# Optimization experiments

Hardware: AMD Instinct MI355X
Metric: run time of the kernel (lower is better)

Reference implementation:

```python
import jax, jax.numpy as jnp
import numpy as np

WS = 8            # window size (square)
HEADS = 16
HEAD_DIM = 32
DIM = 512
NEG_INF = float('-inf')


def _create_mask(ws, disp, upper_lower, left_right):
    size = ws * ws
    m = np.zeros((size, size), dtype=np.float32)
    d = disp
    if upper_lower:
        m[-d * ws:, :-d * ws] = NEG_INF
        m[:-d * ws, -d * ws:] = NEG_INF
    if left_right:
        m = m.reshape(ws, ws, ws, ws)
        m[:, -d:, :, :-d] = NEG_INF
        m[:, :-d, :, -d:] = NEG_INF
        m = m.reshape(size, size)
    return m


def _relative_indices(ws):
    coords = np.array([[x, y] for x in range(ws) for y in range(ws)])  # [ws^2, 2]
    dist = coords[None, :, :] - coords[:, None, :]                      # [ws^2, ws^2, 2]
    dist += ws - 1
    return dist.astype(np.int64)


_REL_IDX = _relative_indices(WS)                      # [64, 64, 2]
_UL_MASK = jnp.asarray(_create_mask(WS, WS // 2, True, False))   # [64, 64]
_LR_MASK = jnp.asarray(_create_mask(WS, WS // 2, False, True))   # [64, 64]


def setup_inputs() -> dict:
    key = jax.random.key(0)
    ks = jax.random.split(key, 5)
    b, n = 16, 64
    return {
        'x': jax.random.normal(ks[0], (b, n, n, DIM), dtype=jnp.float32),
        'w_qkv': jax.random.normal(ks[1], (3 * HEADS * HEAD_DIM, DIM), dtype=jnp.float32) * 0.02,
        'pos_embedding': jax.random.normal(ks[2], (2 * WS - 1, 2 * WS - 1), dtype=jnp.float32),
        'w_out': jax.random.normal(ks[3], (DIM, HEADS * HEAD_DIM), dtype=jnp.float32) * 0.02,
        'b_out': jax.random.normal(ks[4], (DIM,), dtype=jnp.float32) * 0.02,
    }


def reference(x, w_qkv, pos_embedding, w_out, b_out):
    disp = WS // 2
    scale = HEAD_DIM ** -0.5
    b, n_h, n_w, _ = x.shape
    nw_h, nw_w = n_h // WS, n_w // WS

    # cyclic shift (shifted=True)
    x = jnp.roll(x, shift=(-disp, -disp), axis=(1, 2))

    qkv = x @ w_qkv.T                                   # [b, n_h, n_w, 3*h*d]
    qkv = qkv.reshape(b, nw_h, WS, nw_w, WS, 3, HEADS, HEAD_DIM)
    # -> [3, b, heads, n_windows, window_tokens, head_dim]
    qkv = qkv.transpose(5, 0, 6, 1, 3, 2, 4, 7).reshape(
        3, b, HEADS, nw_h * nw_w, WS * WS, HEAD_DIM)
    q, k, v = qkv[0], qkv[1], qkv[2]

    dots = jnp.einsum('bhwid,bhwjd->bhwij', q, k) * scale
    # relative position bias
    dots = dots + pos_embedding[_REL_IDX[:, :, 0], _REL_IDX[:, :, 1]]
    # shift masks: last window-row and last window-column
    dots = dots.at[:, :, -nw_w:].add(_UL_MASK)
    dots = dots.at[:, :, nw_w - 1::nw_w].add(_LR_MASK)

    attn = jax.nn.softmax(dots, axis=-1)
    out = jnp.einsum('bhwij,bhwjd->bhwid', attn, v)     # [b,h,nw,ws^2,d]

    out = out.reshape(b, HEADS, nw_h, nw_w, WS, WS, HEAD_DIM)
    out = out.transpose(0, 2, 4, 3, 5, 1, 6).reshape(b, n_h, n_w, HEADS * HEAD_DIM)
    out = out @ w_out.T + b_out

    out = jnp.roll(out, shift=(disp, disp), axis=(1, 2))
    return out
```

## Files before the change

kernel.cpp:

```cpp
#include <hip/hip_runtime.h>
#include <hip/hip_bf16.h>
#include <stdint.h>

typedef __bf16 bf16;
typedef __attribute__((ext_vector_type(4))) float f32x4;
typedef __attribute__((ext_vector_type(8))) bf16 bf16x8;
typedef __attribute__((ext_vector_type(4))) bf16 bf16x4;

#define AS1 __attribute__((address_space(1)))
#define AS3 __attribute__((address_space(3)))

static __device__ __forceinline__ void gload_lds16(const bf16* g, bf16* l) {
  __builtin_amdgcn_global_load_lds((const AS1 void*)g, (AS3 void*)l, 16, 0, 0);
}

#define BAR __builtin_amdgcn_s_barrier()
#define LGKM0 asm volatile("s_waitcnt lgkmcnt(0)" ::: "memory")
#define VMC(n) asm volatile("s_waitcnt vmcnt(" #n ")" ::: "memory")
#define SCHED0 __builtin_amdgcn_sched_barrier(0)

#define STAGE_A(gsrc, dst, kt_) do {                                          \
  _Pragma("unroll") for (int s_ = 0; s_ < 4; ++s_) {                          \
    int idx_ = s_ * 256 + tid;                                                \
    int r_ = idx_ >> 3, c_ = idx_ & 7;                                        \
    gload_lds16((gsrc) + (size_t)r_ * 512 + ((kt_) << 6) + ((c_ ^ (r_ & 7)) << 3), \
                (dst) + idx_ * 8);                                            \
  }                                                                           \
} while (0)

#define LOADB(ktq, NCOLX) do {                                                \
  const bf16* bp_ = Bptr + (size_t)(ktq) * ((size_t)(NCOLX) * 64);            \
  _Pragma("unroll") for (int cb_ = 0; cb_ < 4; ++cb_)                         \
  _Pragma("unroll") for (int ks_ = 0; ks_ < 2; ++ks_)                         \
    bfr[cb_][ks_] = *(const bf16x8*)(bp_ + cb_ * 128 + (size_t)ks_ * (NCOLX) * 32); \
} while (0)

#define LOADB6(ktq) do {                                                      \
  const bf16* bp_ = Bptr + (size_t)(ktq) * 98304;                             \
  _Pragma("unroll") for (int cb_ = 0; cb_ < 6; ++cb_)                         \
  _Pragma("unroll") for (int ks_ = 0; ks_ < 2; ++ks_)                         \
    bfr[cb_][ks_] = *(const bf16x8*)(bp_ + cb_ * 128 + ks_ * 49152);          \
} while (0)

#define KLOOP_BD(Ag, NCOLX)                                                   \
  f32x4 acc[4][4] = {};                                                       \
  bf16x8 af[4][2], bfr[4][2];                                                 \
  STAGE_A(Ag, SA0, 0);                                                        \
  LOADB(0, NCOLX);                                                            \
  VMC(8); BAR;                                                                \
  STAGE_A(Ag, SA1, 1);                                                        \
  _Pragma("unroll 2")                                                         \
  for (int kt = 0; kt < 8; ++kt) {                                            \
    bf16* Ap = (kt & 1) ? SA1 : SA0;                                          \
    _Pragma("unroll") for (int i_ = 0; i_ < 4; ++i_) {                        \
      int ra_ = wr + i_ * 16 + lr;                                            \
      _Pragma("unroll") for (int ks_ = 0; ks_ < 2; ++ks_)                     \
        af[i_][ks_] = *(const bf16x8*)(Ap + ra_ * 64 + (((ks_ * 4 + lg) ^ (ra_ & 7)) << 3)); \
    }                                                                         \
    LGKM0; SCHED0;                                                            \
    __builtin_amdgcn_s_setprio(1);                                            \
    _Pragma("unroll") for (int i_ = 0; i_ < 4; ++i_)                          \
    _Pragma("unroll") for (int j_ = 0; j_ < 4; ++j_)                          \
    _Pragma("unroll") for (int ks_ = 0; ks_ < 2; ++ks_)                       \
      acc[i_][j_] = __builtin_amdgcn_mfma_f32_16x16x32_bf16(                  \
          af[i_][ks_], bfr[j_][ks_], acc[i_][j_], 0, 0, 0);                   \
    __builtin_amdgcn_s_setprio(0);                                            \
    if (kt < 7) LOADB(kt + 1, NCOLX);                                         \
    if (kt < 7) { VMC(8); }                                                   \
    BAR;                                                                      \
    if (kt < 6) STAGE_A(Ag, Ap, kt + 2);                                      \
  }

__global__ __launch_bounds__(256) void prep_x(const float* __restrict__ x,
                                              bf16* __restrict__ xs) {
  int m = blockIdx.x * 8 + (threadIdx.x >> 5);
  int lane = threadIdx.x & 31;
  int b = m >> 12, win = (m >> 6) & 63, t = m & 63;
  int ip = ((win >> 3) << 3) + (t >> 3);
  int jp = ((win & 7) << 3) + (t & 7);
  int io = (ip + 4) & 63, jo = (jp + 4) & 63;
  const float* src = x + ((((size_t)(b << 6) + io) << 6) + jo) * 512;
  bf16* dst = xs + ((size_t)m << 9);
  #pragma unroll
  for (int c0 = 0; c0 < 512; c0 += 128) {
    int c = c0 + lane * 4;
    float4 v = *(const float4*)(src + c);
    bf16x4 o = { (bf16)v.x, (bf16)v.y, (bf16)v.z, (bf16)v.w };
    *(bf16x4*)(dst + c) = o;
  }
}

__global__ __launch_bounds__(256) void prep_w(const float* __restrict__ wqkv,
                                              const float* __restrict__ wout,
                                              bf16* __restrict__ wqkv_bt,
                                              bf16* __restrict__ wout_bt) {
  int r = blockIdx.x * 8 + (threadIdx.x >> 5);
  int lane = threadIdx.x & 31;
  const float* src;
  bf16* dstb;
  int ncol, col;
  float sc = 1.0f;
  if (r < 1536) {
    int part = r >> 9, h = (r >> 5) & 15, d = r & 31;
    src = wqkv + (size_t)r * 512; dstb = wqkv_bt; ncol = 1536;
    col = h * 96 + part * 32 + d;
    if (part == 0) sc = 0.17677669529663689f;
  } else {
    src = wout + (size_t)(r - 1536) * 512; dstb = wout_bt; ncol = 512; col = r - 1536;
  }
  #pragma unroll
  for (int kb = lane; kb < 64; kb += 32) {
    float4 v0 = *(const float4*)(src + kb * 8);
    float4 v1 = *(const float4*)(src + kb * 8 + 4);
    bf16x8 o = { (bf16)(v0.x * sc), (bf16)(v0.y * sc), (bf16)(v0.z * sc), (bf16)(v0.w * sc),
                 (bf16)(v1.x * sc), (bf16)(v1.y * sc), (bf16)(v1.z * sc), (bf16)(v1.w * sc) };
    *(bf16x8*)(dstb + ((size_t)kb * ncol + col) * 8) = o;
  }
}

__global__ __launch_bounds__(256) void prep_bias(const float* __restrict__ pos,
                                                 float* __restrict__ bias4) {
  for (int idx = threadIdx.x; idx < 4 * 4096; idx += 256) {
    int ty = idx >> 12, ij = idx & 4095;
    int i = ij >> 6, j = ij & 63;
    int rx = ((j >> 3) - (i >> 3)) + 7;
    int ry = ((j & 7) - (i & 7)) + 7;
    float v = pos[rx * 15 + ry];
    if ((ty & 1) && (((i ^ j) >> 5) & 1)) v = -1e30f;
    if ((ty & 2) && (((i ^ j) >> 2) & 1)) v = -1e30f;
    bias4[idx] = v;
  }
}

__global__ __launch_bounds__(256, 2) void qkv_attn(
    const bf16* __restrict__ xs, const bf16* __restrict__ wb2,
    const float* __restrict__ bias4, bf16* __restrict__ ao) {
  __shared__ union { bf16 A[2][8192]; bf16 E[4][4096]; } sm;
  bf16* SA0 = sm.A[0]; bf16* SA1 = sm.A[1];

  const int tid = threadIdx.x, wave = tid >> 6, lane = tid & 63;
  const int ww = wave & 1, wh = wave >> 1;
  const int lr = lane & 15, lg = lane >> 4;

  int bid = blockIdx.x;
  bid = (bid & 7) * 512 + (bid >> 3);
  const int mt = bid >> 3, hp = bid & 7;
  const int h = hp * 2 + wh;

  const bf16* Ag = xs + ((size_t)mt * 128) * 512;
  const bf16* Bptr = wb2 + (((size_t)lg * 1536) + h * 96 + lr) * 8;

  f32x4 acc[4][6] = {};
  bf16x8 af[4][2], bfr[6][2];

  STAGE_A(Ag, SA0, 0);
  LOADB6(0);
  VMC(12); BAR;
  STAGE_A(Ag, SA1, 1);
  #pragma unroll 2
  for (int kt = 0; kt < 8; ++kt) {
    bf16* Ap = (kt & 1) ? SA1 : SA0;
    #pragma unroll
    for (int i_ = 0; i_ < 4; ++i_) {
      int ra_ = ww * 64 + i_ * 16 + lr;
      #pragma unroll
      for (int ks_ = 0; ks_ < 2; ++ks_)
        af[i_][ks_] = *(const bf16x8*)(Ap + ra_ * 64 + (((ks_ * 4 + lg) ^ (ra_ & 7)) << 3));
    }
    LGKM0; SCHED0;
    __builtin_amdgcn_s_setprio(1);
    #pragma unroll
    for (int i_ = 0; i_ < 4; ++i_)
      #pragma unroll
      for (int j_ = 0; j_ < 6; ++j_)
        #pragma unroll
        for (int ks_ = 0; ks_ < 2; ++ks_)
          acc[i_][j_] = __builtin_amdgcn_mfma_f32_16x16x32_bf16(
              af[i_][ks_], bfr[j_][ks_], acc[i_][j_], 0, 0, 0);
    __builtin_amdgcn_s_setprio(0);
    if (kt < 7) { LOADB6(kt + 1); VMC(12); }
    BAR;
    if (kt < 6) STAGE_A(Ag, Ap, kt + 2);
  }
  bf16* Ew = sm.E[wave];
  #pragma unroll
  for (int i = 0; i < 4; ++i)
    #pragma unroll
    for (int r = 0; r < 4; ++r) {
      int row = i * 16 + (lg << 2) + r;
      #pragma unroll
      for (int j = 0; j < 4; ++j) {
        int c = j * 16 + lr;
        Ew[row * 64 + (c ^ ((row & 7) << 3))] = (bf16)acc[i][j][r];
      }
    }
  bf16x8 vf[2][2];
  {
    const int s0 = lr + 16 * ((2 * lg) & 3);
    const int s1 = lr + 16 * ((2 * lg + 1) & 3);
    const bool lo = (lg < 2);
    #pragma unroll
    for (int kk = 0; kk < 2; ++kk)
      #pragma unroll
      for (int nj = 0; nj < 2; ++nj) {
        float f[8];
        #pragma unroll
        for (int c = 0; c < 4; ++c) {
          float a0 = __shfl(acc[2 * kk][4 + nj][c], s0);
          float a1 = __shfl(acc[2 * kk + 1][4 + nj][c], s0);
          f[c] = lo ? a0 : a1;
          float b0 = __shfl(acc[2 * kk][4 + nj][c], s1);
          float b1 = __shfl(acc[2 * kk + 1][4 + nj][c], s1);
          f[4 + c] = lo ? b0 : b1;
        }
        vf[kk][nj] = (bf16x8){ (bf16)f[0], (bf16)f[1], (bf16)f[2], (bf16)f[3],
                               (bf16)f[4], (bf16)f[5], (bf16)f[6], (bf16)f[7] };
      }
  }
  LGKM0; SCHED0;
  bf16x8 qf[4], kf[4];
  #pragma unroll
  for (int i = 0; i < 4; ++i) {
    int ra = i * 16 + lr;
    qf[i] = *(const bf16x8*)(Ew + ra * 64 + (((lg << 3)) ^ ((ra & 7) << 3)));
    kf[i] = *(const bf16x8*)(Ew + ra * 64 + ((32 + (lg << 3)) ^ ((ra & 7) << 3)));
  }
  f32x4 s[4][4] = {};
  #pragma unroll
  for (int i = 0; i < 4; ++i)
    #pragma unroll
    for (int j = 0; j < 4; ++j)
      s[i][j] = __builtin_amdgcn_mfma_f32_16x16x32_bf16(qf[i], kf[j], s[i][j], 0, 0, 0);

  const int gw = mt * 2 + ww;
  const int win = gw & 63;
  const int ty = ((win >= 56) ? 1 : 0) | (((win & 7) == 7) ? 2 : 0);
  const float* bt = bias4 + ty * 4096;
  #pragma unroll
  for (int i = 0; i < 4; ++i)
    #pragma unroll
    for (int r = 0; r < 4; ++r) {
      int row = i * 16 + (lg << 2) + r;
      #pragma unroll
      for (int j = 0; j < 4; ++j)
        s[i][j][r] += bt[row * 64 + j * 16 + lr];
    }
  #pragma unroll
  for (int i = 0; i < 4; ++i)
    #pragma unroll
    for (int r = 0; r < 4; ++r) {
      float mx = fmaxf(fmaxf(s[i][0][r], s[i][1][r]), fmaxf(s[i][2][r], s[i][3][r]));
      mx = fmaxf(mx, __shfl_xor(mx, 1));
      mx = fmaxf(mx, __shfl_xor(mx, 2));
      mx = fmaxf(mx, __shfl_xor(mx, 4));
      mx = fmaxf(mx, __shfl_xor(mx, 8));
      float sum = 0.f;
      #pragma unroll
      for (int j = 0; j < 4; ++j) { s[i][j][r] = __expf(s[i][j][r] - mx); sum += s[i][j][r]; }
      sum += __shfl_xor(sum, 1);
      sum += __shfl_xor(sum, 2);
      sum += __shfl_xor(sum, 4);
      sum += __shfl_xor(sum, 8);
      float inv = 1.0f / sum;
      int row = i * 16 + (lg << 2) + r;
      #pragma unroll
      for (int j = 0; j < 4; ++j) {
        int c = j * 16 + lr;
        Ew[row * 64 + (c ^ ((row & 7) << 3))] = (bf16)(s[i][j][r] * inv);
      }
    }
  LGKM0; SCHED0;
  f32x4 o[4][2] = {};
  #pragma unroll
  for (int kk = 0; kk < 2; ++kk)
    #pragma unroll
    for (int mi = 0; mi < 4; ++mi) {
      int ra = mi * 16 + lr;
      bf16x8 pa = *(const bf16x8*)(Ew + ra * 64 + ((kk * 32 + (lg << 3)) ^ ((ra & 7) << 3)));
      #pragma unroll
      for (int nj = 0; nj < 2; ++nj)
        o[mi][nj] = __builtin_amdgcn_mfma_f32_16x16x32_bf16(pa, vf[kk][nj], o[mi][nj], 0, 0, 0);
    }
  bf16* dst = ao + ((size_t)(mt * 128 + ww * 64)) * 512 + h * 32;
  #pragma unroll
  for (int mi = 0; mi < 4; ++mi)
    #pragma unroll
    for (int r = 0; r < 4; ++r) {
      int t = mi * 16 + (lg << 2) + r;
      #pragma unroll
      for (int nj = 0; nj < 2; ++nj)
        dst[(size_t)t * 512 + nj * 16 + lr] = (bf16)o[mi][nj][r];
    }
}

__global__ __launch_bounds__(256, 3) void gemm_out(
    const bf16* __restrict__ ao, const bf16* __restrict__ wob,
    const float* __restrict__ bout, float* __restrict__ out) {
  __shared__ bf16 SA[2][8192];
  bf16* SA0 = SA[0]; bf16* SA1 = SA[1];

  const int tid = threadIdx.x, wave = tid >> 6, lane = tid & 63;
  int bid = blockIdx.x;
  bid = (bid & 7) * 256 + (bid >> 3);
  const int mt = bid >> 2, nt = bid & 3;
  const bf16* Ag = ao + ((size_t)mt * 128) * 512;
  const int wr = (wave >> 1) << 6, wc = (wave & 1) << 6;
  const int lr = lane & 15, lg = lane >> 4;
  const bf16* Bptr = wob + (((size_t)lg * 512) + nt * 128 + wc + lr) * 8;

  KLOOP_BD(Ag, 512)

  float bv[4];
  #pragma unroll
  for (int j = 0; j < 4; ++j) bv[j] = bout[nt * 128 + wc + j * 16 + lr];
  #pragma unroll
  for (int i = 0; i < 4; ++i)
    #pragma unroll
    for (int r = 0; r < 4; ++r) {
      int m = (mt << 7) + wr + i * 16 + (lg << 2) + r;
      int b = m >> 12, win = (m >> 6) & 63, t = m & 63;
      int ip = ((win >> 3) << 3) + (t >> 3);
      int jp = ((win & 7) << 3) + (t & 7);
      int io = (ip + 4) & 63, jo = (jp + 4) & 63;
      float* orow = out + ((((size_t)(b << 6) + io) << 6) + jo) * 512 + nt * 128 + wc;
      #pragma unroll
      for (int j = 0; j < 4; ++j)
        orow[j * 16 + lr] = acc[i][j][r] + bv[j];
    }
}

extern "C" void kernel_launch(void* const* d_in, const int* in_sizes, int n_in,
                              void* d_out, int out_size, void* d_ws, size_t ws_size,
                              hipStream_t stream) {
  const float* x    = (const float*)d_in[0];
  const float* wqkv = (const float*)d_in[1];
  const float* pos  = (const float*)d_in[2];
  const float* wout = (const float*)d_in[3];
  const float* bout = (const float*)d_in[4];
  float* out = (float*)d_out;

  char* ws = (char*)d_ws;
  bf16* xs      = (bf16*)(ws);
  bf16* ao      = (bf16*)(ws + 67108864);
  bf16* wqkv_bt = (bf16*)(ws + 268435456);
  bf16* wout_bt = (bf16*)(ws + 270008320);
  float* bias4  = (float*)(ws + 270532608);

  prep_x<<<dim3(8192), dim3(256), 0, stream>>>(x, xs);
  prep_w<<<dim3(256), dim3(256), 0, stream>>>(wqkv, wout, wqkv_bt, wout_bt);
  prep_bias<<<dim3(1), dim3(256), 0, stream>>>(pos, bias4);
  qkv_attn<<<dim3(4096), dim3(256), 0, stream>>>(xs, wqkv_bt, bias4, ao);
  gemm_out<<<dim3(2048), dim3(256), 0, stream>>>(ao, wout_bt, bout, out);
}
```

Before: 261.8 us.

## Deepen QKV GEMM pipeline with 4-slot LDS ring and split B-fragment prefetch

Replaces the double-buffered A staging in the fused QKV-attention kernel with a 4-slot LDS ring that stages three k-tiles ahead. The loop is fully unrolled with ping-pong A fragment registers, so the next tile's LDS reads are issued before the current MFMAs. The B fragment load is split into two halves, so each half's global load for the next k-tile overlaps the MFMAs on the other half. It uses fine-grained vmcnt/lgkmcnt waits to hide global and LDS latency, at the cost of doubled LDS (64KB) and more registers, which could reduce occupancy below two blocks per CU.

```diff
diff --git a/kernel.cpp b/kernel.cpp
--- a/kernel.cpp
+++ b/kernel.cpp
@@ -15,9 +15,12 @@
 }
 
 #define BAR __builtin_amdgcn_s_barrier()
-#define LGKM0 asm volatile("s_waitcnt lgkmcnt(0)" ::: "memory")
-#define VMC(n) asm volatile("s_waitcnt vmcnt(" #n ")" ::: "memory")
 #define SCHED0 __builtin_amdgcn_sched_barrier(0)
+#define VMC_(n) asm volatile("s_waitcnt vmcnt(" #n ")" ::: "memory")
+#define VMC(n) VMC_(n)
+#define LGKM_(n) asm volatile("s_waitcnt lgkmcnt(" #n ")" ::: "memory")
+#define LGKM(n) LGKM_(n)
+#define LGKM0 LGKM(0)
 
 #define STAGE_A(gsrc, dst, kt_) do {                                          \
   _Pragma("unroll") for (int s_ = 0; s_ < 4; ++s_) {                          \
@@ -33,13 +36,6 @@
   _Pragma("unroll") for (int cb_ = 0; cb_ < 4; ++cb_)                         \
   _Pragma("unroll") for (int ks_ = 0; ks_ < 2; ++ks_)                         \
     bfr[cb_][ks_] = *(const bf16x8*)(bp_ + cb_ * 128 + (size_t)ks_ * (NCOLX) * 32); \
-} while (0)
-
-#define LOADB6(ktq) do {                                                      \
-  const bf16* bp_ = Bptr + (size_t)(ktq) * 98304;                             \
-  _Pragma("unroll") for (int cb_ = 0; cb_ < 6; ++cb_)                         \
-  _Pragma("unroll") for (int ks_ = 0; ks_ < 2; ++ks_)                         \
-    bfr[cb_][ks_] = *(const bf16x8*)(bp_ + cb_ * 128 + ks_ * 49152);          \
 } while (0)
 
 #define KLOOP_BD(Ag, NCOLX)                                                   \
@@ -132,11 +128,50 @@
   }
 }
 
+#define SR(s) (smb + (s) * 8192)
+
+#define STAGE_R(slot, kt_) STAGE_A(Ag, SR(slot), kt_)
+
+#define RD_AF(dst, sptr) do {                                                 \
+  _Pragma("unroll") for (int i_ = 0; i_ < 4; ++i_) {                          \
+    int ra_ = ww * 64 + i_ * 16 + lr;                                         \
+    _Pragma("unroll") for (int ks_ = 0; ks_ < 2; ++ks_)                       \
+      dst[i_][ks_] = *(const bf16x8*)((sptr) + ra_ * 64 + (((ks_ * 4 + lg) ^ (ra_ & 7)) << 3)); \
+  }                                                                           \
+} while (0)
+
+#define LOADB_H(set, ktq, hf) do {                                            \
+  const bf16* bp_ = Bptr + (size_t)(ktq) * 98304 + (hf) * 384;                \
+  _Pragma("unroll") for (int cb_ = 0; cb_ < 3; ++cb_)                         \
+  _Pragma("unroll") for (int ks_ = 0; ks_ < 2; ++ks_)                         \
+    set[cb_][ks_] = *(const bf16x8*)(bp_ + cb_ * 128 + ks_ * 49152);          \
+} while (0)
+
+#define MMP(afs, bs, j0)                                                      \
+  _Pragma("unroll") for (int i_ = 0; i_ < 4; ++i_)                            \
+  _Pragma("unroll") for (int jj_ = 0; jj_ < 3; ++jj_)                         \
+  _Pragma("unroll") for (int ks_ = 0; ks_ < 2; ++ks_)                         \
+    acc[i_][(j0) + jj_] = __builtin_amdgcn_mfma_f32_16x16x32_bf16(            \
+        afs[i_][ks_], bs[jj_][ks_], acc[i_][(j0) + jj_], 0, 0, 0);
+
+#define KT_BODY(CUR, NXT, KT, CN, FN, LN) do {                                \
+  if ((KT) < 7) RD_AF(NXT, SR(((KT) + 1) & 3));                               \
+  if ((KT) <= 4) STAGE_R(((KT) + 3) & 3, (KT) + 3);                           \
+  VMC(CN); LGKM(LN); SCHED0;                                                  \
+  __builtin_amdgcn_s_setprio(1); MMP(CUR, bfrX, 0);                           \
+  __builtin_amdgcn_s_setprio(0);                                              \
+  if ((KT) < 7) LOADB_H(bfrX, (KT) + 1, 0);                                   \
+  VMC(FN); SCHED0;                                                            \
+  __builtin_amdgcn_s_setprio(1); MMP(CUR, bfrY, 3);                           \
+  __builtin_amdgcn_s_setprio(0);                                              \
+  if ((KT) < 7) LOADB_H(bfrY, (KT) + 1, 1);                                   \
+  if ((KT) < 7) BAR;                                                          \
+} while (0)
+
 __global__ __launch_bounds__(256, 2) void qkv_attn(
     const bf16* __restrict__ xs, const bf16* __restrict__ wb2,
     const float* __restrict__ bias4, bf16* __restrict__ ao) {
-  __shared__ union { bf16 A[2][8192]; bf16 E[4][4096]; } sm;
-  bf16* SA0 = sm.A[0]; bf16* SA1 = sm.A[1];
+  __shared__ bf16 smb[32768];
 
   const int tid = threadIdx.x, wave = tid >> 6, lane = tid & 63;
   const int ww = wave & 1, wh = wave >> 1;
@@ -151,38 +186,23 @@
   const bf16* Bptr = wb2 + (((size_t)lg * 1536) + h * 96 + lr) * 8;
 
   f32x4 acc[4][6] = {};
-  bf16x8 af[4][2], bfr[6][2];
-
-  STAGE_A(Ag, SA0, 0);
-  LOADB6(0);
-  VMC(12); BAR;
-  STAGE_A(Ag, SA1, 1);
-  #pragma unroll 2
-  for (int kt = 0; kt < 8; ++kt) {
-    bf16* Ap = (kt & 1) ? SA1 : SA0;
-    #pragma unroll
-    for (int i_ = 0; i_ < 4; ++i_) {
-      int ra_ = ww * 64 + i_ * 16 + lr;
-      #pragma unroll
-      for (int ks_ = 0; ks_ < 2; ++ks_)
-        af[i_][ks_] = *(const bf16x8*)(Ap + ra_ * 64 + (((ks_ * 4 + lg) ^ (ra_ & 7)) << 3));
-    }
-    LGKM0; SCHED0;
-    __builtin_amdgcn_s_setprio(1);
-    #pragma unroll
-    for (int i_ = 0; i_ < 4; ++i_)
-      #pragma unroll
-      for (int j_ = 0; j_ < 6; ++j_)
-        #pragma unroll
-        for (int ks_ = 0; ks_ < 2; ++ks_)
-          acc[i_][j_] = __builtin_amdgcn_mfma_f32_16x16x32_bf16(
-              af[i_][ks_], bfr[j_][ks_], acc[i_][j_], 0, 0, 0);
-    __builtin_amdgcn_s_setprio(0);
-    if (kt < 7) { LOADB6(kt + 1); VMC(12); }
-    BAR;
-    if (kt < 6) STAGE_A(Ag, Ap, kt + 2);
-  }
-  bf16* Ew = sm.E[wave];
+  bf16x8 afA[4][2], afB[4][2], bfrX[3][2], bfrY[3][2];
+
+  STAGE_R(0, 0); STAGE_R(1, 1); STAGE_R(2, 2);
+  LOADB_H(bfrX, 0, 0); LOADB_H(bfrY, 0, 1);
+  VMC(16); BAR;
+  RD_AF(afA, SR(0));
+
+  KT_BODY(afA, afB, 0, 10, 10, 8);
+  KT_BODY(afB, afA, 1, 10, 10, 8);
+  KT_BODY(afA, afB, 2, 10, 10, 8);
+  KT_BODY(afB, afA, 3, 10, 10, 8);
+  KT_BODY(afA, afB, 4, 10, 10, 8);
+  KT_BODY(afB, afA, 5, 6, 6, 8);
+  KT_BODY(afA, afB, 6, 6, 6, 8);
+  KT_BODY(afB, afA, 7, 6, 0, 0);
+
+  bf16* Ew = smb + wave * 4096;
   #pragma unroll
   for (int i = 0; i < 4; ++i)
     #pragma unroll
```

After: 250.9 us. 4.1% less time.

## Split qkv_attn per head across waves, halving per-wave rows and raising occupancy

Applied to the files above, without the earlier changes.

Each block now handles one head instead of two. The four waves split into two windows by two 32-row halves, so per-wave accumulators halve and the launch bound rises to 3 blocks per CU, with the grid doubled. V is now written transposed to LDS and read back for the PV matmul, replacing the cross-lane shuffle transposition. This adds block barriers, because K and V are shared between the two row-half waves. It also doubles the A-tile staging traffic, since x is reloaded once per head rather than once per head pair.

```diff
diff --git a/kernel.cpp b/kernel.cpp
--- a/kernel.cpp
+++ b/kernel.cpp
@@ -15,9 +15,10 @@
 }
 
 #define BAR __builtin_amdgcn_s_barrier()
+#define SCHED0 __builtin_amdgcn_sched_barrier(0)
+#define VMC_(n) asm volatile("s_waitcnt vmcnt(" #n ")" ::: "memory")
+#define VMC(n) VMC_(n)
 #define LGKM0 asm volatile("s_waitcnt lgkmcnt(0)" ::: "memory")
-#define VMC(n) asm volatile("s_waitcnt vmcnt(" #n ")" ::: "memory")
-#define SCHED0 __builtin_amdgcn_sched_barrier(0)
 
 #define STAGE_A(gsrc, dst, kt_) do {                                          \
   _Pragma("unroll") for (int s_ = 0; s_ < 4; ++s_) {                          \
@@ -132,26 +133,25 @@
   }
 }
 
-__global__ __launch_bounds__(256, 2) void qkv_attn(
+__global__ __launch_bounds__(256, 3) void qkv_attn(
     const bf16* __restrict__ xs, const bf16* __restrict__ wb2,
     const float* __restrict__ bias4, bf16* __restrict__ ao) {
-  __shared__ union { bf16 A[2][8192]; bf16 E[4][4096]; } sm;
-  bf16* SA0 = sm.A[0]; bf16* SA1 = sm.A[1];
+  __shared__ bf16 smb[16384];
+  bf16* SA0 = smb; bf16* SA1 = smb + 8192;
 
   const int tid = threadIdx.x, wave = tid >> 6, lane = tid & 63;
-  const int ww = wave & 1, wh = wave >> 1;
+  const int ww = wave >> 1, rh = wave & 1;
   const int lr = lane & 15, lg = lane >> 4;
 
   int bid = blockIdx.x;
-  bid = (bid & 7) * 512 + (bid >> 3);
-  const int mt = bid >> 3, hp = bid & 7;
-  const int h = hp * 2 + wh;
+  bid = (bid & 7) * 1024 + (bid >> 3);
+  const int mt = bid >> 4, h = bid & 15;
 
   const bf16* Ag = xs + ((size_t)mt * 128) * 512;
   const bf16* Bptr = wb2 + (((size_t)lg * 1536) + h * 96 + lr) * 8;
 
-  f32x4 acc[4][6] = {};
-  bf16x8 af[4][2], bfr[6][2];
+  f32x4 acc[2][6] = {};
+  bf16x8 af[2][2], bfr[6][2];
 
   STAGE_A(Ag, SA0, 0);
   LOADB6(0);
@@ -161,8 +161,8 @@
   for (int kt = 0; kt < 8; ++kt) {
     bf16* Ap = (kt & 1) ? SA1 : SA0;
     #pragma unroll
-    for (int i_ = 0; i_ < 4; ++i_) {
-      int ra_ = ww * 64 + i_ * 16 + lr;
+    for (int i_ = 0; i_ < 2; ++i_) {
+      int ra_ = ww * 64 + rh * 32 + i_ * 16 + lr;
       #pragma unroll
       for (int ks_ = 0; ks_ < 2; ++ks_)
         af[i_][ks_] = *(const bf16x8*)(Ap + ra_ * 64 + (((ks_ * 4 + lg) ^ (ra_ & 7)) << 3));
@@ -170,7 +170,7 @@
     LGKM0; SCHED0;
     __builtin_amdgcn_s_setprio(1);
     #pragma unroll
-    for (int i_ = 0; i_ < 4; ++i_)
+    for (int i_ = 0; i_ < 2; ++i_)
       #pragma unroll
       for (int j_ = 0; j_ < 6; ++j_)
         #pragma unroll
@@ -182,52 +182,41 @@
     BAR;
     if (kt < 6) STAGE_A(Ag, Ap, kt + 2);
   }
-  bf16* Ew = sm.E[wave];
-  #pragma unroll
-  for (int i = 0; i < 4; ++i)
-    #pragma unroll
-    for (int r = 0; r < 4; ++r) {
-      int row = i * 16 + (lg << 2) + r;
+
+  bf16* Eu = smb + ww * 6144;
+  bf16* Ev = Eu + 4096;
+  #pragma unroll
+  for (int i = 0; i < 2; ++i)
+    #pragma unroll
+    for (int r = 0; r < 4; ++r) {
+      int row = rh * 32 + i * 16 + (lg << 2) + r;
       #pragma unroll
       for (int j = 0; j < 4; ++j) {
         int c = j * 16 + lr;
-        Ew[row * 64 + (c ^ ((row & 7) << 3))] = (bf16)acc[i][j][r];
+        Eu[row * 64 + (c ^ ((row & 7) << 3))] = (bf16)acc[i][j][r];
       }
-    }
-  bf16x8 vf[2][2];
-  {
-    const int s0 = lr + 16 * ((2 * lg) & 3);
-    const int s1 = lr + 16 * ((2 * lg + 1) & 3);
-    const bool lo = (lg < 2);
-    #pragma unroll
-    for (int kk = 0; kk < 2; ++kk)
-      #pragma unroll
-      for (int nj = 0; nj < 2; ++nj) {
-        float f[8];
-        #pragma unroll
-        for (int c = 0; c < 4; ++c) {
-          float a0 = __shfl(acc[2 * kk][4 + nj][c], s0);
-          float a1 = __shfl(acc[2 * kk + 1][4 + nj][c], s0);
-          f[c] = lo ? a0 : a1;
-          float b0 = __shfl(acc[2 * kk][4 + nj][c], s1);
-          float b1 = __shfl(acc[2 * kk + 1][4 + nj][c], s1);
-          f[4 + c] = lo ? b0 : b1;
-        }
-        vf[kk][nj] = (bf16x8){ (bf16)f[0], (bf16)f[1], (bf16)f[2], (bf16)f[3],
-                               (bf16)f[4], (bf16)f[5], (bf16)f[6], (bf16)f[7] };
+      #pragma unroll
+      for (int j = 4; j < 6; ++j) {
+        int cv = (j - 4) * 16 + lr;
+        Ev[cv * 64 + (row ^ ((cv & 7) << 3))] = (bf16)acc[i][j][r];
       }
-  }
-  LGKM0; SCHED0;
-  bf16x8 qf[4], kf[4];
-  #pragma unroll
-  for (int i = 0; i < 4; ++i) {
-    int ra = i * 16 + lr;
-    qf[i] = *(const bf16x8*)(Ew + ra * 64 + (((lg << 3)) ^ ((ra & 7) << 3)));
-    kf[i] = *(const bf16x8*)(Ew + ra * 64 + ((32 + (lg << 3)) ^ ((ra & 7) << 3)));
-  }
-  f32x4 s[4][4] = {};
-  #pragma unroll
-  for (int i = 0; i < 4; ++i)
+    }
+  LGKM0; BAR;
+
+  bf16x8 qf[2], kf[4];
+  #pragma unroll
+  for (int i = 0; i < 2; ++i) {
+    int ra = rh * 32 + i * 16 + lr;
+    qf[i] = *(const bf16x8*)(Eu + ra * 64 + ((lg << 3) ^ ((ra & 7) << 3)));
+  }
+  #pragma unroll
+  for (int j = 0; j < 4; ++j) {
+    int rb = j * 16 + lr;
+    kf[j] = *(const bf16x8*)(Eu + rb * 64 + ((32 + (lg << 3)) ^ ((rb & 7) << 3)));
+  }
+  f32x4 s[2][4] = {};
+  #pragma unroll
+  for (int i = 0; i < 2; ++i)
     #pragma unroll
     for (int j = 0; j < 4; ++j)
       s[i][j] = __builtin_amdgcn_mfma_f32_16x16x32_bf16(qf[i], kf[j], s[i][j], 0, 0, 0);
@@ -237,16 +226,16 @@
   const int ty = ((win >= 56) ? 1 : 0) | (((win & 7) == 7) ? 2 : 0);
   const float* bt = bias4 + ty * 4096;
   #pragma unroll
-  for (int i = 0; i < 4; ++i)
-    #pragma unroll
-    for (int r = 0; r < 4; ++r) {
-      int row = i * 16 + (lg << 2) + r;
+  for (int i = 0; i < 2; ++i)
+    #pragma unroll
+    for (int r = 0; r < 4; ++r) {
+      int grow = rh * 32 + i * 16 + (lg << 2) + r;
       #pragma unroll
       for (int j = 0; j < 4; ++j)
-        s[i][j][r] += bt[row * 64 + j * 16 + lr];
-    }
-  #pragma unroll
-  for (int i = 0; i < 4; ++i)
+        s[i][j][r] += bt[grow * 64 + j * 16 + lr];
+    }
+  #pragma unroll
+  for (int i = 0; i < 2; ++i)
     #pragma unroll
     for (int r = 0; r < 4; ++r) {
       float mx = fmaxf(fmaxf(s[i][0][r], s[i][1][r]), fmaxf(s[i][2][r], s[i][3][r]));
@@ -262,31 +251,47 @@
       sum += __shfl_xor(sum, 4);
       sum += __shfl_xor(sum, 8);
       float inv = 1.0f / sum;
-      int row = i * 16 + (lg << 2) + r;
+      #pragma unroll
+      for (int j = 0; j < 4; ++j) s[i][j][r] *= inv;
+    }
+  BAR;
+  #pragma unroll
+  for (int i = 0; i < 2; ++i)
+    #pragma unroll
+    for (int r = 0; r < 4; ++r) {
+      int row = rh * 32 + i * 16 + (lg << 2) + r;
       #pragma unroll
       for (int j = 0; j < 4; ++j) {
         int c = j * 16 + lr;
-        Ew[row * 64 + (c ^ ((row & 7) << 3))] = (bf16)(s[i][j][r] * inv);
+        Eu[row * 64 + (c ^ ((row & 7) << 3))] = (bf16)s[i][j][r];
       }
     }
   LGKM0; SCHED0;
-  f32x4 o[4][2] = {};
+  bf16x8 vf[2][2];
   #pragma unroll
   for (int kk = 0; kk < 2; ++kk)
     #pragma unroll
-    for (int mi = 0; mi < 4; ++mi) {
-      int ra = mi * 16 + lr;
-      bf16x8 pa = *(const bf16x8*)(Ew + ra * 64 + ((kk * 32 + (lg << 3)) ^ ((ra & 7) << 3)));
+    for (int nj = 0; nj < 2; ++nj) {
+      int dv = nj * 16 + lr;
+      vf[kk][nj] = *(const bf16x8*)(Ev + dv * 64 + ((kk * 32 + (lg << 3)) ^ ((dv & 7) << 3)));
+    }
+  f32x4 o[2][2] = {};
+  #pragma unroll
+  for (int kk = 0; kk < 2; ++kk)
+    #pragma unroll
+    for (int mi = 0; mi < 2; ++mi) {
+      int ra = rh * 32 + mi * 16 + lr;
+      bf16x8 pa = *(const bf16x8*)(Eu + ra * 64 + ((kk * 32 + (lg << 3)) ^ ((ra & 7) << 3)));
       #pragma unroll
       for (int nj = 0; nj < 2; ++nj)
         o[mi][nj] = __builtin_amdgcn_mfma_f32_16x16x32_bf16(pa, vf[kk][nj], o[mi][nj], 0, 0, 0);
     }
   bf16* dst = ao + ((size_t)(mt * 128 + ww * 64)) * 512 + h * 32;
   #pragma unroll
-  for (int mi = 0; mi < 4; ++mi)
-    #pragma unroll
-    for (int r = 0; r < 4; ++r) {
-      int t = mi * 16 + (lg << 2) + r;
+  for (int mi = 0; mi < 2; ++mi)
+    #pragma unroll
+    for (int r = 0; r < 4; ++r) {
+      int t = rh * 32 + mi * 16 + (lg << 2) + r;
       #pragma unroll
       for (int nj = 0; nj < 2; ++nj)
         dst[(size_t)t * 512 + nj * 16 + lr] = (bf16)o[mi][nj][r];
@@ -349,6 +354,6 @@
   prep_x<<<dim3(8192), dim3(256), 0, stream>>>(x, xs);
   prep_w<<<dim3(256), dim3(256), 0, stream>>>(wqkv, wout, wqkv_bt, wout_bt);
   prep_bias<<<dim3(1), dim3(256), 0, stream>>>(pos, bias4);
-  qkv_attn<<<dim3(4096), dim3(256), 0, stream>>>(xs, wqkv_bt, bias4, ao);
+  qkv_attn<<<dim3(8192), dim3(256), 0, stream>>>(xs, wqkv_bt, bias4, ao);
   gemm_out<<<dim3(2048), dim3(256), 0, stream>>>(ao, wout_bt, bout, out);
 }
```

Measured after the change: 275.3 us. 5.2% more time.
